# Optimization experiments

Hardware: AMD Instinct MI355X
Metric: run time of the kernel (lower is better)

The kernel has to match this reference:

```python
import jax, jax.numpy as jnp
import numpy as np

B, H, W, C = 32, 56, 56, 192
WS, SHIFT, NH = 7, 3, 6
HD = C // NH
N = WS * WS
NW = (H // WS) * (W // WS)
SCALE = HD ** -0.5
EPS = 1e-5


def _layer_norm(x, g, b):
    mu = jnp.mean(x, axis=-1, keepdims=True)
    var = jnp.mean(jnp.square(x - mu), axis=-1, keepdims=True)
    return (x - mu) * jax.lax.rsqrt(var + EPS) * g + b


def _relative_position_index():
    coords = np.stack(np.meshgrid(np.arange(WS), np.arange(WS), indexing='ij'))  # [2,ws,ws]
    coords = coords.reshape(2, -1)                                               # [2,N]
    rel = coords[:, :, None] - coords[:, None, :]                                # [2,N,N]
    rel = rel.transpose(1, 2, 0).astype(np.int64)
    rel[..., 0] += WS - 1
    rel[..., 1] += WS - 1
    rel[..., 0] *= 2 * WS - 1
    return jnp.asarray(rel.sum(-1))  # [N,N]


def _attn_mask():
    img = np.zeros((H, W), dtype=np.float32)
    cnt = 0
    slices = (slice(0, -WS), slice(-WS, -SHIFT), slice(-SHIFT, None))
    for hs in slices:
        for ws_ in slices:
            img[hs, ws_] = cnt
            cnt += 1
    mw = img.reshape(H // WS, WS, W // WS, WS).transpose(0, 2, 1, 3).reshape(-1, N)  # [nW,N]
    diff = mw[:, :, None] - mw[:, None, :]
    return jnp.asarray(np.where(diff != 0, -100.0, 0.0).astype(np.float32))  # [nW,N,N]


REL_IDX = _relative_position_index()
ATTN_MASK = _attn_mask()


def setup_inputs() -> dict:
    key = jax.random.key(0)
    ks = jax.random.split(key, 16)
    s = 0.02
    return {
        'x': jax.random.normal(ks[0], (B, H * W, C), jnp.float32),
        'ln1_g': jnp.ones((C,), jnp.float32),
        'ln1_b': jnp.zeros((C,), jnp.float32),
        'qkv_w': jax.random.normal(ks[1], (3 * C, C), jnp.float32) * s,
        'qkv_b': jnp.zeros((3 * C,), jnp.float32),
        'proj_w': jax.random.normal(ks[2], (C, C), jnp.float32) * s,
        'proj_b': jnp.zeros((C,), jnp.float32),
        'rpb_table': jax.random.normal(ks[3], ((2 * WS - 1) ** 2, NH), jnp.float32) * s,
        'ln2_g': jnp.ones((C,), jnp.float32),
        'ln2_b': jnp.zeros((C,), jnp.float32),
        'fc1_w': jax.random.normal(ks[4], (4 * C, C), jnp.float32) * s,
        'fc1_b': jnp.zeros((4 * C,), jnp.float32),
        'fc2_w': jax.random.normal(ks[5], (C, 4 * C), jnp.float32) * s,
        'fc2_b': jnp.zeros((C,), jnp.float32),
    }


def reference(x, ln1_g, ln1_b, qkv_w, qkv_b, proj_w, proj_b, rpb_table,
              ln2_g, ln2_b, fc1_w, fc1_b, fc2_w, fc2_b):
    shortcut = x
    h = _layer_norm(x, ln1_g, ln1_b).reshape(B, H, W, C)
    # cyclic shift
    h = jnp.roll(h, (-SHIFT, -SHIFT), axis=(1, 2))
    # window partition -> [B*nW, N, C]
    h = h.reshape(B, H // WS, WS, W // WS, WS, C).transpose(0, 1, 3, 2, 4, 5)
    h = h.reshape(B * NW, N, C)
    # qkv
    qkv = h @ qkv_w.T + qkv_b                                   # [Bn,N,3C]
    qkv = qkv.reshape(B * NW, N, 3, NH, HD).transpose(2, 0, 3, 1, 4)
    q, k, v = qkv[0], qkv[1], qkv[2]                             # [Bn,nh,N,hd]
    attn = jnp.einsum('bhnd,bhmd->bhnm', q * SCALE, k)           # [Bn,nh,N,N]
    # relative position bias
    bias = rpb_table[REL_IDX.reshape(-1)].reshape(N, N, NH).transpose(2, 0, 1)
    attn = attn + bias[None]
    # shift mask
    attn = attn.reshape(B, NW, NH, N, N) + ATTN_MASK[None, :, None]
    attn = jax.nn.softmax(attn.reshape(B * NW, NH, N, N), axis=-1)
    h = jnp.einsum('bhnm,bhmd->bhnd', attn, v)                   # [Bn,nh,N,hd]
    h = h.transpose(0, 2, 1, 3).reshape(B * NW, N, C)
    h = h @ proj_w.T + proj_b
    # window reverse + reverse shift
    h = h.reshape(B, H // WS, W // WS, WS, WS, C).transpose(0, 1, 3, 2, 4, 5)
    h = h.reshape(B, H, W, C)
    h = jnp.roll(h, (SHIFT, SHIFT), axis=(1, 2)).reshape(B, H * W, C)
    x = shortcut + h
    # MLP
    m = _layer_norm(x, ln2_g, ln2_b)
    m = jax.nn.gelu(m @ fc1_w.T + fc1_b, approximate=False)
    m = m @ fc2_w.T + fc2_b
    return x + m
```

## Files before the change

kernel.cpp:

```cpp
#include <hip/hip_runtime.h>
#include <hip/hip_bf16.h>
#include <cstdint>
#include <cstddef>

typedef __hip_bfloat16 bf16;
using f32x4  = __attribute__((ext_vector_type(4))) float;
using bf16x8 = __attribute__((ext_vector_type(8))) short;

#define DEVI __device__ __forceinline__

DEVI int reg3(int u) { return (u < 49) ? 0 : ((u < 53) ? 1 : 2); }

DEVI unsigned short f2bu(float v) {
  bf16 b = __float2bfloat16(v);
  return *reinterpret_cast<unsigned short*>(&b);
}

DEVI float gelu_f(float v) {
  const float y = 0.7978845608028654f * (v + 0.044715f * v * v * v);
  const float e = __expf(2.0f * y);
  const float th = 1.0f - 2.0f / (e + 1.0f);
  return 0.5f * v * (1.0f + th);
}

DEVI void gload_lds16(const void* g, void* l) {
  __builtin_amdgcn_global_load_lds(
      (const __attribute__((address_space(1))) unsigned int*)g,
      (__attribute__((address_space(3))) unsigned int*)l, 16, 0, 0);
}

__global__ __launch_bounds__(256) void cvt_kernel(const float* __restrict__ src,
                                                  bf16* __restrict__ dst, int n)
{
  const int i = blockIdx.x * 256 + threadIdx.x;
  if (i < n) dst[i] = __float2bfloat16(src[i]);
}

template<bool PERM>
__global__ __launch_bounds__(256) void ln_kernel(const float* __restrict__ x,
                                                 const float* __restrict__ gw,
                                                 const float* __restrict__ bw,
                                                 bf16* __restrict__ out,
                                                 int grow0)
{
  const int lane = threadIdx.x & 63;
  const int ridx = blockIdx.x * 4 + (threadIdx.x >> 6);
  size_t src;
  if (PERM) {
    const int g   = grow0 + ridx;
    const int wid = g / 49;
    const int nn  = g - wid * 49;
    const int b_  = wid >> 6, wim = wid & 63;
    const int wy  = wim >> 3, wx = wim & 7;
    const int ny  = nn / 7,  nx = nn - (nn / 7) * 7;
    int i = wy * 7 + ny + 3; if (i >= 56) i -= 56;
    int j = wx * 7 + nx + 3; if (j >= 56) j -= 56;
    src = (size_t)(b_ * 3136 + i * 56 + j);
  } else {
    src = (size_t)ridx;
  }
  const float* xr = x + src * 192;
  float v0 = xr[lane];
  float v1 = xr[lane + 64];
  float v2 = xr[lane + 128];
  float s = v0 + v1 + v2;
#pragma unroll
  for (int off = 32; off > 0; off >>= 1) s += __shfl_xor(s, off);
  const float mu = s * (1.0f / 192.0f);
  const float d0 = v0 - mu, d1 = v1 - mu, d2 = v2 - mu;
  float vs = d0 * d0 + d1 * d1 + d2 * d2;
#pragma unroll
  for (int off = 32; off > 0; off >>= 1) vs += __shfl_xor(vs, off);
  const float rstd = rsqrtf(vs * (1.0f / 192.0f) + 1e-5f);
  bf16* orow = out + (size_t)ridx * 192;
  orow[lane]       = __float2bfloat16(d0 * rstd * gw[lane]       + bw[lane]);
  orow[lane + 64]  = __float2bfloat16(d1 * rstd * gw[lane + 64]  + bw[lane + 64]);
  orow[lane + 128] = __float2bfloat16(d2 * rstd * gw[lane + 128] + bw[lane + 128]);
}

template<int MODE>
__global__ __launch_bounds__(512, 4) void gemm_kernel(const bf16* __restrict__ A,
                                                      const bf16* __restrict__ Bt,
                                                      const float* __restrict__ bias,
                                                      const float* __restrict__ resid,
                                                      void* __restrict__ outv,
                                                      int N, int K, int grow0)
{
  __shared__ short lds[2][128 * 64 + 192 * 64];
  const int tid  = threadIdx.x;
  const int lane = tid & 63;
  const int w    = tid >> 6;
  const int wm   = (w >> 2) * 64;
  const int wn   = (w & 3) * 48;
  const int m0   = blockIdx.y * 128;
  const int n0   = blockIdx.x * 192;
  const int lrow = lane >> 3;
  const int lseg = lane & 7;
  const int ksw  = (lseg * 8) ^ (lrow << 3);

  f32x4 acc[4][3];
#pragma unroll
  for (int i = 0; i < 4; i++)
#pragma unroll
    for (int j = 0; j < 3; j++) acc[i][j] = (f32x4){0.f, 0.f, 0.f, 0.f};

  const int nk = K >> 6;

  auto issue = [&](int buf, int kt) {
    const int k0 = kt << 6;
    short* LA = &lds[buf][0];
    short* LB = &lds[buf][128 * 64];
#pragma unroll
    for (int i = 0; i < 2; i++) {
      const int chunk = w * 2 + i;
      gload_lds16(A + (size_t)(m0 + chunk * 8 + lrow) * K + (k0 + ksw), LA + chunk * 512);
    }
#pragma unroll
    for (int i = 0; i < 3; i++) {
      const int chunk = w * 3 + i;
      gload_lds16(Bt + (size_t)(n0 + chunk * 8 + lrow) * K + (k0 + ksw), LB + chunk * 512);
    }
  };

  issue(0, 0);
  __syncthreads();

  for (int kt = 0; kt < nk; kt++) {
    const int buf = kt & 1;
    if (kt + 1 < nk) issue(buf ^ 1, kt + 1);
    const char* LA = (const char*)&lds[buf][0];
    const char* LB = (const char*)&lds[buf][128 * 64];
#pragma unroll
    for (int kk = 0; kk < 2; kk++) {
      bf16x8 af[4], bg[3];
#pragma unroll
      for (int mf = 0; mf < 4; mf++) {
        const int row = wm + mf * 16 + (lane & 15);
        const int kb  = (kk * 64 + ((lane >> 4) << 4)) ^ ((row & 7) << 4);
        af[mf] = *(const bf16x8*)(LA + row * 128 + kb);
      }
#pragma unroll
      for (int nf = 0; nf < 3; nf++) {
        const int row = wn + nf * 16 + (lane & 15);
        const int kb  = (kk * 64 + ((lane >> 4) << 4)) ^ ((row & 7) << 4);
        bg[nf] = *(const bf16x8*)(LB + row * 128 + kb);
      }
#pragma unroll
      for (int mf = 0; mf < 4; mf++)
#pragma unroll
        for (int nf = 0; nf < 3; nf++)
          acc[mf][nf] = __builtin_amdgcn_mfma_f32_16x16x32_bf16(af[mf], bg[nf], acc[mf][nf], 0, 0, 0);
    }
    __syncthreads();
  }

  float bv[3];
  int ncol[3];
#pragma unroll
  for (int nf = 0; nf < 3; nf++) {
    ncol[nf] = n0 + wn + nf * 16 + (lane & 15);
    bv[nf]   = bias[ncol[nf]];
  }
#pragma unroll
  for (int mf = 0; mf < 4; mf++) {
#pragma unroll
    for (int r = 0; r < 4; r++) {
      const int m = m0 + wm + mf * 16 + ((lane >> 4) << 2) + r;
      if constexpr (MODE == 1) {
        const int gm  = grow0 + m;
        const int wid = gm / 49;
        const int nn  = gm - wid * 49;
        const int b_  = wid >> 6, wim = wid & 63;
        const int wy  = wim >> 3, wx = wim & 7;
        const int ny  = nn / 7, nx = nn - (nn / 7) * 7;
        int i = wy * 7 + ny + 3; if (i >= 56) i -= 56;
        int j = wx * 7 + nx + 3; if (j >= 56) j -= 56;
        const size_t t = (size_t)(b_ * 3136 + i * 56 + j) * 192;
        float* O = (float*)outv;
#pragma unroll
        for (int nf = 0; nf < 3; nf++)
          O[t + ncol[nf]] = acc[mf][nf][r] + bv[nf] + resid[t + ncol[nf]];
      } else if constexpr (MODE == 3) {
        float* O = (float*)outv + (size_t)m * N;
#pragma unroll
        for (int nf = 0; nf < 3; nf++)
          O[ncol[nf]] = acc[mf][nf][r] + bv[nf] + O[ncol[nf]];
      } else {
        bf16* O = (bf16*)outv + (size_t)m * N;
#pragma unroll
        for (int nf = 0; nf < 3; nf++) {
          float v = acc[mf][nf][r] + bv[nf];
          if constexpr (MODE == 2) v = gelu_f(v);
          O[ncol[nf]] = __float2bfloat16(v);
        }
      }
    }
  }
}

__global__ __launch_bounds__(64) void attn_kernel(const bf16* __restrict__ qkv,
                                                  const float* __restrict__ rpb,
                                                  bf16* __restrict__ aout)
{
  __shared__ unsigned short Vt[32 * 64];
  __shared__ unsigned short Pl[64 * 64];
  __shared__ float Bl[169];
  const int lane = threadIdx.x;
  const int wid  = blockIdx.x;
  const int h    = blockIdx.y;
  const unsigned short* qkvu = (const unsigned short*)qkv;
  const size_t base = (size_t)wid * 49 * 576 + h * 32;

#pragma unroll
  for (int i = 0; i < 3; i++) {
    const int idx = lane + 64 * i;
    if (idx < 169) Bl[idx] = rpb[idx * 6 + h];
  }
#pragma unroll
  for (int i = 0; i < 8; i++)
    ((unsigned long long*)Vt)[lane + 64 * i] = 0ull;

#pragma unroll
  for (int it = 0; it < 7; it++) {
    const int idx = lane + 64 * it;
    if (idx < 392) {
      const int n  = idx >> 3;
      const int d0 = (idx & 7) * 4;
      ushort4 v = *(const ushort4*)(qkvu + base + (size_t)n * 576 + 384 + d0);
      Vt[(d0 + 0) * 64 + (n ^ (((d0 + 0) & 7) << 3))] = v.x;
      Vt[(d0 + 1) * 64 + (n ^ (((d0 + 1) & 7) << 3))] = v.y;
      Vt[(d0 + 2) * 64 + (n ^ (((d0 + 2) & 7) << 3))] = v.z;
      Vt[(d0 + 3) * 64 + (n ^ (((d0 + 3) & 7) << 3))] = v.w;
    }
  }

  bf16x8 qf[4], kf[4];
#pragma unroll
  for (int t = 0; t < 4; t++) {
    int rq = (lane & 15) + t * 16; if (rq > 48) rq = 48;
    qf[t] = *(const bf16x8*)(qkvu + base + (size_t)rq * 576 + ((lane >> 4) * 8));
    kf[t] = *(const bf16x8*)(qkvu + base + (size_t)rq * 576 + 192 + ((lane >> 4) * 8));
  }

  f32x4 s[4][4];
#pragma unroll
  for (int mt = 0; mt < 4; mt++)
#pragma unroll
    for (int nt = 0; nt < 4; nt++)
      s[mt][nt] = __builtin_amdgcn_mfma_f32_16x16x32_bf16(qf[mt], kf[nt],
                    (f32x4){0.f, 0.f, 0.f, 0.f}, 0, 0, 0);

  const int wim = wid & 63;
  const int wy = wim >> 3, wx = wim & 7;
  int labn[4], ch[4], cw[4];
  bool cval[4];
#pragma unroll
  for (int nt = 0; nt < 4; nt++) {
    const int C = (lane & 15) + nt * 16;
    cval[nt] = (C < 49);
    const int cc = cval[nt] ? C : 48;
    ch[nt] = cc / 7; cw[nt] = cc - ch[nt] * 7;
    labn[nt] = reg3(wy * 7 + ch[nt]) * 3 + reg3(wx * 7 + cw[nt]);
  }

#pragma unroll
  for (int mt = 0; mt < 4; mt++) {
    f32x4 rm, sm, inv;
#pragma unroll
    for (int r = 0; r < 4; r++) {
      int R = mt * 16 + ((lane >> 4) << 2) + r; if (R > 48) R = 48;
      const int mh = R / 7, mw = R - (R / 7) * 7;
      const int labm = reg3(wy * 7 + mh) * 3 + reg3(wx * 7 + mw);
#pragma unroll
      for (int nt = 0; nt < 4; nt++) {
        float sv = s[mt][nt][r] * 0.1767766953f
                 + Bl[(mh - ch[nt] + 6) * 13 + (mw - cw[nt] + 6)];
        if (labn[nt] != labm) sv -= 100.f;
        if (!cval[nt]) sv = -3e38f;
        s[mt][nt][r] = sv;
      }
      rm[r] = fmaxf(fmaxf(s[mt][0][r], s[mt][1][r]), fmaxf(s[mt][2][r], s[mt][3][r]));
    }
#pragma unroll
    for (int mk = 1; mk < 16; mk <<= 1)
#pragma unroll
      for (int r = 0; r < 4; r++) rm[r] = fmaxf(rm[r], __shfl_xor(rm[r], mk));
#pragma unroll
    for (int r = 0; r < 4; r++) {
      float acc = 0.f;
#pragma unroll
      for (int nt = 0; nt < 4; nt++) {
        const float p = __expf(s[mt][nt][r] - rm[r]);
        s[mt][nt][r] = p;
        acc += p;
      }
      sm[r] = acc;
    }
#pragma unroll
    for (int mk = 1; mk < 16; mk <<= 1)
#pragma unroll
      for (int r = 0; r < 4; r++) sm[r] += __shfl_xor(sm[r], mk);
#pragma unroll
    for (int r = 0; r < 4; r++) inv[r] = 1.0f / sm[r];
#pragma unroll
    for (int nt = 0; nt < 4; nt++)
#pragma unroll
      for (int r = 0; r < 4; r++) {
        const int R = mt * 16 + ((lane >> 4) << 2) + r;
        const int C = (lane & 15) + nt * 16;
        Pl[R * 64 + (C ^ ((R & 7) << 3))] = f2bu(s[mt][nt][r] * inv[r]);
      }
  }

  f32x4 o[4][2];
#pragma unroll
  for (int mt = 0; mt < 4; mt++)
#pragma unroll
    for (int n2 = 0; n2 < 2; n2++) o[mt][n2] = (f32x4){0.f, 0.f, 0.f, 0.f};
#pragma unroll
  for (int kk = 0; kk < 2; kk++) {
    const int kb = kk * 64 + ((lane >> 4) << 4);
    bf16x8 vb[2];
#pragma unroll
    for (int n2 = 0; n2 < 2; n2++) {
      const int d = (lane & 15) + n2 * 16;
      vb[n2] = *(const bf16x8*)((const char*)Vt + d * 128 + (kb ^ ((d & 7) << 4)));
    }
#pragma unroll
    for (int mt = 0; mt < 4; mt++) {
      const int R = (lane & 15) + mt * 16;
      const bf16x8 pa = *(const bf16x8*)((const char*)Pl + R * 128 + (kb ^ ((R & 7) << 4)));
#pragma unroll
      for (int n2 = 0; n2 < 2; n2++)
        o[mt][n2] = __builtin_amdgcn_mfma_f32_16x16x32_bf16(pa, vb[n2], o[mt][n2], 0, 0, 0);
    }
  }

#pragma unroll
  for (int mt = 0; mt < 4; mt++)
#pragma unroll
    for (int r = 0; r < 4; r++) {
      const int R = mt * 16 + ((lane >> 4) << 2) + r;
      if (R < 49) {
        bf16* orow = aout + (size_t)(wid * 49 + R) * 192 + h * 32;
#pragma unroll
        for (int n2 = 0; n2 < 2; n2++)
          orow[n2 * 16 + (lane & 15)] = __float2bfloat16(o[mt][n2][r]);
      }
    }
}

extern "C" void kernel_launch(void* const* d_in, const int* in_sizes, int n_in,
                              void* d_out, int out_size, void* d_ws, size_t ws_size,
                              hipStream_t stream)
{
  (void)in_sizes; (void)n_in; (void)out_size;
  const float* x     = (const float*)d_in[0];
  const float* ln1g  = (const float*)d_in[1];
  const float* ln1b  = (const float*)d_in[2];
  const float* qkvw  = (const float*)d_in[3];
  const float* qkvb  = (const float*)d_in[4];
  const float* projw = (const float*)d_in[5];
  const float* projb = (const float*)d_in[6];
  const float* rpb   = (const float*)d_in[7];
  const float* ln2g  = (const float*)d_in[8];
  const float* ln2b  = (const float*)d_in[9];
  const float* fc1w  = (const float*)d_in[10];
  const float* fc1b  = (const float*)d_in[11];
  const float* fc2w  = (const float*)d_in[12];
  const float* fc2b  = (const float*)d_in[13];
  float* out = (float*)d_out;
  char* ws   = (char*)d_ws;

  bf16* wqkv = (bf16*)(ws);
  bf16* wproj = (bf16*)(ws + 221184);
  bf16* wfc1 = (bf16*)(ws + 294912);
  bf16* wfc2 = (bf16*)(ws + 589824);
  cvt_kernel<<<dim3(432), dim3(256), 0, stream>>>(qkvw, wqkv, 110592);
  cvt_kernel<<<dim3(144), dim3(256), 0, stream>>>(projw, wproj, 36864);
  cvt_kernel<<<dim3(576), dim3(256), 0, stream>>>(fc1w, wfc1, 147456);
  cvt_kernel<<<dim3(576), dim3(256), 0, stream>>>(fc2w, wfc2, 147456);

  char* cws = ws + 884736;
  const size_t avail = (ws_size > 884736ull) ? ws_size - 884736ull : 0;

  int Bc = 32;
  while (Bc > 2 && (size_t)Bc * 4816896ull > avail) Bc >>= 1;
  const int nb = 32 / Bc;
  bf16* qkv_c  = (bf16*)cws;
  bf16* hwin_c = (bf16*)(cws + (size_t)Bc * 3612672ull);

  for (int c = 0; c < nb; c++) {
    const int R0 = c * Bc * 3136;
    const int Mc = Bc * 3136;
    ln_kernel<true><<<dim3(Mc / 4), dim3(256), 0, stream>>>(x, ln1g, ln1b, hwin_c, R0);
    gemm_kernel<0><<<dim3(3, Mc / 128), dim3(512), 0, stream>>>(hwin_c, wqkv, qkvb, nullptr, qkv_c, 576, 192, 0);
    attn_kernel<<<dim3(Bc * 64, 6), dim3(64), 0, stream>>>(qkv_c, rpb, hwin_c);
    gemm_kernel<1><<<dim3(1, Mc / 128), dim3(512), 0, stream>>>(hwin_c, wproj, projb, x, out, 192, 192, R0);
  }

  int Rc = 100352;
  while (Rc > 6272 && (size_t)Rc * 1920ull > avail) Rc >>= 1;
  bf16* ln2_c = (bf16*)cws;
  bf16* a1_c  = (bf16*)(cws + (size_t)Rc * 384ull);

  for (int r0 = 0; r0 < 100352; r0 += Rc) {
    ln_kernel<false><<<dim3(Rc / 4), dim3(256), 0, stream>>>(out + (size_t)r0 * 192, ln2g, ln2b, ln2_c, 0);
    gemm_kernel<2><<<dim3(4, Rc / 128), dim3(512), 0, stream>>>(ln2_c, wfc1, fc1b, nullptr, a1_c, 768, 192, 0);
    gemm_kernel<3><<<dim3(1, Rc / 128), dim3(512), 0, stream>>>(a1_c, wfc2, fc2b, nullptr, out + (size_t)r0 * 192, 192, 768, 0);
  }
}
```

Measured before the change: 378.4 us.

## Add persistent K=192 GEMM keeping weight tile resident in LDS

Introduces a persistent GEMM kernel for the K=192 projections (qkv, proj, fc1). Each block loads its full 192x192 weight slice into LDS once, then loops over 64-row A tiles with double-buffered async staging. The aim is to stop reloading weights for every tile and to overlap A loads with MFMA work. In exchange it uses about 120KB of LDS, which limits each CU to one block, and the fixed grid sizes (170/256/128) may leave CUs unevenly loaded. The original gemm kernel is reduced to the fc2 path only.

New measurement: 374.9 us. Within noise of the previous version (-0.9%).

```diff
diff --git a/kernel.cpp b/kernel.cpp
--- a/kernel.cpp
+++ b/kernel.cpp
@@ -79,6 +79,128 @@
 }
 
 template<int MODE>
+__global__ __launch_bounds__(512) void pgemm_kernel(const bf16* __restrict__ A,
+                                                    const bf16* __restrict__ Bt,
+                                                    const float* __restrict__ bias,
+                                                    const float* __restrict__ resid,
+                                                    void* __restrict__ outv,
+                                                    int N, int grow0, int MT)
+{
+  __shared__ short Bp[192 * 192];
+  __shared__ short La[2][64 * 192];
+  const int tid  = threadIdx.x;
+  const int lane = tid & 63;
+  const int w    = tid >> 6;
+  const int wm   = (w >> 2) * 32;
+  const int wn   = (w & 3) * 48;
+  const int np   = blockIdx.x;
+  const int n0   = np * 192;
+  const int G    = gridDim.y;
+  const int g    = blockIdx.y;
+  const int kq   = lane >> 4;
+
+#pragma unroll
+  for (int i = 0; i < 9; i++) {
+    const int chunk = w * 9 + i;
+    const int idx = chunk * 64 + lane;
+    const int row = idx / 24;
+    const int seg = idx - row * 24;
+    const int ksrc = (seg * 8) ^ ((row & 7) << 3);
+    gload_lds16(Bt + (size_t)(n0 + row) * 192 + ksrc, Bp + chunk * 512);
+  }
+
+  auto stageA = [&](int buf, int mt) {
+    const int m0 = mt * 64;
+#pragma unroll
+    for (int i = 0; i < 3; i++) {
+      const int chunk = w * 3 + i;
+      const int idx = chunk * 64 + lane;
+      const int row = idx / 24;
+      const int seg = idx - row * 24;
+      const int ksrc = (seg * 8) ^ ((row & 7) << 3);
+      gload_lds16(A + (size_t)(m0 + row) * 192 + ksrc, &La[buf][0] + chunk * 512);
+    }
+  };
+
+  int buf = 0;
+  stageA(0, g < MT ? g : 0);
+  __syncthreads();
+
+  for (int mt = g; mt < MT; mt += G) {
+    if (mt + G < MT) stageA(buf ^ 1, mt + G);
+    const char* LA = (const char*)&La[buf][0];
+
+    f32x4 acc[2][3];
+#pragma unroll
+    for (int i = 0; i < 2; i++)
+#pragma unroll
+      for (int j = 0; j < 3; j++) acc[i][j] = (f32x4){0.f, 0.f, 0.f, 0.f};
+
+#pragma unroll
+    for (int kk = 0; kk < 6; kk++) {
+      const int q = kk * 64 + (kq << 4);
+      bf16x8 af[2], bg[3];
+#pragma unroll
+      for (int mf = 0; mf < 2; mf++) {
+        const int ar = wm + mf * 16 + (lane & 15);
+        af[mf] = *(const bf16x8*)(LA + ar * 384 + (q ^ ((ar & 7) << 4)));
+      }
+#pragma unroll
+      for (int nf = 0; nf < 3; nf++) {
+        const int br = wn + nf * 16 + (lane & 15);
+        bg[nf] = *(const bf16x8*)((const char*)Bp + br * 384 + (q ^ ((br & 7) << 4)));
+      }
+#pragma unroll
+      for (int mf = 0; mf < 2; mf++)
+#pragma unroll
+        for (int nf = 0; nf < 3; nf++)
+          acc[mf][nf] = __builtin_amdgcn_mfma_f32_16x16x32_bf16(af[mf], bg[nf], acc[mf][nf], 0, 0, 0);
+    }
+
+    const int m0 = mt * 64;
+    float bv[3];
+    int ncol[3];
+#pragma unroll
+    for (int nf = 0; nf < 3; nf++) {
+      ncol[nf] = n0 + wn + nf * 16 + (lane & 15);
+      bv[nf]   = bias[ncol[nf]];
+    }
+#pragma unroll
+    for (int mf = 0; mf < 2; mf++) {
+#pragma unroll
+      for (int r = 0; r < 4; r++) {
+        const int m = m0 + wm + mf * 16 + ((lane >> 4) << 2) + r;
+        if constexpr (MODE == 1) {
+          const int gm  = grow0 + m;
+          const int wid = gm / 49;
+          const int nn  = gm - wid * 49;
+          const int b_  = wid >> 6, wim = wid & 63;
+          const int wy  = wim >> 3, wx = wim & 7;
+          const int ny  = nn / 7, nx = nn - (nn / 7) * 7;
+          int i = wy * 7 + ny + 3; if (i >= 56) i -= 56;
+          int j = wx * 7 + nx + 3; if (j >= 56) j -= 56;
+          const size_t t = (size_t)(b_ * 3136 + i * 56 + j) * 192;
+          float* O = (float*)outv;
+#pragma unroll
+          for (int nf = 0; nf < 3; nf++)
+            O[t + ncol[nf]] = acc[mf][nf][r] + bv[nf] + resid[t + ncol[nf]];
+        } else {
+          bf16* O = (bf16*)outv + (size_t)m * N;
+#pragma unroll
+          for (int nf = 0; nf < 3; nf++) {
+            float v = acc[mf][nf][r] + bv[nf];
+            if constexpr (MODE == 2) v = gelu_f(v);
+            O[ncol[nf]] = __float2bfloat16(v);
+          }
+        }
+      }
+    }
+    __syncthreads();
+    buf ^= 1;
+  }
+}
+
+template<int MODE>
 __global__ __launch_bounds__(512, 4) void gemm_kernel(const bf16* __restrict__ A,
                                                       const bf16* __restrict__ Bt,
                                                       const float* __restrict__ bias,
@@ -166,34 +288,10 @@
 #pragma unroll
     for (int r = 0; r < 4; r++) {
       const int m = m0 + wm + mf * 16 + ((lane >> 4) << 2) + r;
-      if constexpr (MODE == 1) {
-        const int gm  = grow0 + m;
-        const int wid = gm / 49;
-        const int nn  = gm - wid * 49;
-        const int b_  = wid >> 6, wim = wid & 63;
-        const int wy  = wim >> 3, wx = wim & 7;
-        const int ny  = nn / 7, nx = nn - (nn / 7) * 7;
-        int i = wy * 7 + ny + 3; if (i >= 56) i -= 56;
-        int j = wx * 7 + nx + 3; if (j >= 56) j -= 56;
-        const size_t t = (size_t)(b_ * 3136 + i * 56 + j) * 192;
-        float* O = (float*)outv;
-#pragma unroll
-        for (int nf = 0; nf < 3; nf++)
-          O[t + ncol[nf]] = acc[mf][nf][r] + bv[nf] + resid[t + ncol[nf]];
-      } else if constexpr (MODE == 3) {
-        float* O = (float*)outv + (size_t)m * N;
-#pragma unroll
-        for (int nf = 0; nf < 3; nf++)
-          O[ncol[nf]] = acc[mf][nf][r] + bv[nf] + O[ncol[nf]];
-      } else {
-        bf16* O = (bf16*)outv + (size_t)m * N;
-#pragma unroll
-        for (int nf = 0; nf < 3; nf++) {
-          float v = acc[mf][nf][r] + bv[nf];
-          if constexpr (MODE == 2) v = gelu_f(v);
-          O[ncol[nf]] = __float2bfloat16(v);
-        }
-      }
+      float* O = (float*)outv + (size_t)m * N;
+#pragma unroll
+      for (int nf = 0; nf < 3; nf++)
+        O[ncol[nf]] = acc[mf][nf][r] + bv[nf] + O[ncol[nf]];
     }
   }
 }
@@ -393,10 +491,11 @@
   for (int c = 0; c < nb; c++) {
     const int R0 = c * Bc * 3136;
     const int Mc = Bc * 3136;
+    const int MT = Mc / 64;
     ln_kernel<true><<<dim3(Mc / 4), dim3(256), 0, stream>>>(x, ln1g, ln1b, hwin_c, R0);
-    gemm_kernel<0><<<dim3(3, Mc / 128), dim3(512), 0, stream>>>(hwin_c, wqkv, qkvb, nullptr, qkv_c, 576, 192, 0);
+    pgemm_kernel<0><<<dim3(3, 170), dim3(512), 0, stream>>>(hwin_c, wqkv, qkvb, nullptr, qkv_c, 576, 0, MT);
     attn_kernel<<<dim3(Bc * 64, 6), dim3(64), 0, stream>>>(qkv_c, rpb, hwin_c);
-    gemm_kernel<1><<<dim3(1, Mc / 128), dim3(512), 0, stream>>>(hwin_c, wproj, projb, x, out, 192, 192, R0);
+    pgemm_kernel<1><<<dim3(1, 256), dim3(512), 0, stream>>>(hwin_c, wproj, projb, x, out, 192, R0, MT);
   }
 
   int Rc = 100352;
@@ -406,7 +505,7 @@
 
   for (int r0 = 0; r0 < 100352; r0 += Rc) {
     ln_kernel<false><<<dim3(Rc / 4), dim3(256), 0, stream>>>(out + (size_t)r0 * 192, ln2g, ln2b, ln2_c, 0);
-    gemm_kernel<2><<<dim3(4, Rc / 128), dim3(512), 0, stream>>>(ln2_c, wfc1, fc1b, nullptr, a1_c, 768, 192, 0);
+    pgemm_kernel<2><<<dim3(4, 128), dim3(512), 0, stream>>>(ln2_c, wfc1, fc1b, nullptr, a1_c, 768, 0, Rc / 64);
     gemm_kernel<3><<<dim3(1, Rc / 128), dim3(512), 0, stream>>>(a1_c, wfc2, fc2b, nullptr, out + (size_t)r0 * 192, 192, 768, 0);
   }
 }
```
